# Performance work log

Hardware: AMD Instinct MI355X
Metric: run time of the kernel (lower is better)

## Reference

```python
import jax, jax.numpy as jnp
import numpy as np

BIN = (4, 4)
BN_EPS = 1e-5


def patch_split(t, bin_size):
    # b c (bh rh) (bw rw) -> b (bh bw) rh rw c
    B, C, H, W = t.shape
    bh, bw = bin_size
    rH, rW = H // bh, W // bw
    t = t.reshape(B, C, bh, rH, bw, rW)
    t = jnp.transpose(t, (0, 2, 4, 3, 5, 1))
    return t.reshape(B, bh * bw, rH, rW, C)


def patch_recover(t, bin_size):
    # b (bh bw) rh rw c -> b c (bh rh) (bw rw)
    B, N, rH, rW, C = t.shape
    bh, bw = bin_size
    t = t.reshape(B, bh, bw, rH, rW, C)
    t = jnp.transpose(t, (0, 5, 1, 3, 2, 4))
    return t.reshape(B, C, bh * rH, bw * rW)


def setup_inputs() -> dict:
    key = jax.random.key(0)
    ks = jax.random.split(key, 12)
    B, C, H, W = 4, 512, 128, 128
    Ci = C // 2
    bins = BIN[0] * BIN[1]
    s = lambda fan: 1.0 / np.sqrt(fan)
    return {
        "x": jax.random.normal(ks[0], (B, C, H, W), jnp.float32),
        "w_cam": jax.random.normal(ks[1], (C, C), jnp.float32) * s(C),
        "b_cam": jnp.zeros((C,), jnp.float32),
        "w_gcn1": jax.random.normal(ks[2], (bins, bins), jnp.float32) * s(bins),
        "w_gcn2": jax.random.normal(ks[3], (C, C), jnp.float32) * s(C),
        "w_fuse": jax.random.normal(ks[4], (bins,), jnp.float32) * s(bins),
        "b_fuse": jnp.zeros((1,), jnp.float32),
        "w_q": jax.random.normal(ks[5], (Ci, C), jnp.float32) * s(C),
        "b_q": jnp.zeros((Ci,), jnp.float32),
        "w_k": jax.random.normal(ks[6], (Ci, C), jnp.float32) * s(C),
        "b_k": jnp.zeros((Ci,), jnp.float32),
        "w_v": jax.random.normal(ks[7], (Ci, C), jnp.float32) * s(C),
        "b_v": jnp.zeros((Ci,), jnp.float32),
        "w_out": jax.random.normal(ks[8], (C, Ci), jnp.float32) * s(Ci),
        "bn_gamma": jnp.ones((C,), jnp.float32),
        "bn_beta": jnp.zeros((C,), jnp.float32),
        "bn_mean": jnp.zeros((C,), jnp.float32),
        "bn_var": jnp.ones((C,), jnp.float32),
    }


def reference(x, w_cam, b_cam, w_gcn1, w_gcn2, w_fuse, b_fuse,
              w_q, b_q, w_k, b_k, w_v, b_v, w_out,
              bn_gamma, bn_beta, bn_mean, bn_var):
    B, C, H, W = x.shape
    bh, bw = BIN
    bins = bh * bw
    rH, rW = H // bh, W // bw
    P = rH * rW
    K = w_cam.shape[0]  # num_classes == C

    # conv_cam: 1x1 conv (dropout is identity in eval mode)
    cam = jnp.einsum('bchw,kc->bkhw', x, w_cam) + b_cam[None, :, None, None]

    # adaptive avg pool to (bh, bw) then sigmoid
    pooled = cam.reshape(B, K, bh, rH, bw, rW).mean(axis=(3, 5))  # [B,K,bh,bw]
    cls_score = jax.nn.sigmoid(pooled)

    residual = x
    cam_p = patch_split(cam, BIN).reshape(B, bins, P, K)
    x_p = patch_split(x, BIN).reshape(B, bins, P, C)

    # bin confidence: [B, bins, K, 1]
    bin_conf = jnp.transpose(cls_score.reshape(B, K, bins), (0, 2, 1))[..., None]
    pixel_conf = jax.nn.softmax(cam_p, axis=2)  # softmax over pixels in bin

    # local_feats: [B, bins, K, C]
    local = jnp.einsum('bnpk,bnpc->bnkc', pixel_conf, x_p) * bin_conf

    # GCN over bin (node) dimension
    g = jnp.einsum('nm,bmkc->bnkc', w_gcn1, local)
    g = jax.nn.relu(g + local)
    local_feats = jnp.einsum('bnkc,dc->bnkd', g, w_gcn2)

    # fuse: 1x1 conv bins->1, relu -> global feats [B, K, C]
    glob = jnp.einsum('m,bmkc->bkc', w_fuse, local_feats) + b_fuse[0]
    glob = jax.nn.relu(glob)

    # QKV (no scale applied in original forward)
    query = jnp.einsum('bnpc,ic->bnpi', x_p, w_q) + b_q
    key_t = jnp.einsum('bnkc,ic->bnki', local_feats, w_k) + b_k
    value = jnp.einsum('bkc,ic->bki', glob, w_v) + b_v  # shared across bins

    aff = jnp.einsum('bnpi,bnki->bnpk', query, key_t)
    aff = jax.nn.softmax(aff, axis=-1)
    out = jnp.einsum('bnpk,bki->bnpi', aff, value)  # [B, bins, P, Ci]

    Ci = value.shape[-1]
    out = out.reshape(B, bins, rH, rW, Ci)
    out = patch_recover(out, BIN)  # [B, Ci, H, W]

    # conv_out: 1x1 conv (no bias) + BN (eval) + ReLU
    y = jnp.einsum('bihw,ci->bchw', out, w_out)
    inv = jax.lax.rsqrt(bn_var + BN_EPS)
    y = (y - bn_mean[None, :, None, None]) * (bn_gamma * inv)[None, :, None, None] \
        + bn_beta[None, :, None, None]
    y = jax.nn.relu(y)
    return residual + y
```

## Files before the change

### kernel.cpp

```cpp
#include <hip/hip_runtime.h>
#include <hip/hip_bf16.h>
#include <stdint.h>


typedef __attribute__((ext_vector_type(8))) short bfrag;
typedef __attribute__((ext_vector_type(4))) float ffrag;
typedef __hip_bfloat16 bf16;

__device__ __forceinline__ void load_lds16(const void* g, void* l) {
    __builtin_amdgcn_global_load_lds(
        (const __attribute__((address_space(1))) void*)(uintptr_t)g,
        (__attribute__((address_space(3))) void*)(uintptr_t)l,
        16, 0, 0);
}

__global__ void __launch_bounds__(256) gemm_bf16(
    const short* __restrict__ A, int aBatch,
    const short* __restrict__ B, int bBatch, int bShift,
    short* __restrict__ C, int cBatch,
    int M, int N, int K,
    const float* __restrict__ biasM, const float* __restrict__ biasN,
    const float* __restrict__ scaleM)
{
    __shared__ short As[128 * 64];
    __shared__ short Bs[128 * 64];
    const int t = threadIdx.x;
    const int w = t >> 6, lane = t & 63;
    const int bt = blockIdx.z;
    const int m0 = blockIdx.y * 128, n0 = blockIdx.x * 128;
    const short* gA = A + (size_t)bt * aBatch;
    const short* gB = B + (size_t)(bt >> bShift) * bBatch;
    const int wm = w >> 1, wn = w & 1;

    ffrag acc[4][4] = {};

    const int rowbase = w * 32;
    const int lr = lane >> 3;
    const int lc = lane & 7;

    for (int k0 = 0; k0 < K; k0 += 64) {
#pragma unroll
        for (int j = 0; j < 4; ++j) {
            const int rr = rowbase + j * 8 + lr;
            const int ch = lc ^ (rr & 7);
            load_lds16(gA + (size_t)(m0 + rr) * K + k0 + ch * 8,
                       &As[(rowbase + j * 8) * 64]);
            load_lds16(gB + (size_t)(n0 + rr) * K + k0 + ch * 8,
                       &Bs[(rowbase + j * 8) * 64]);
        }
        __syncthreads();
#pragma unroll
        for (int kk = 0; kk < 2; ++kk) {
            bfrag af[4], bfv[4];
#pragma unroll
            for (int i = 0; i < 4; ++i) {
                const int ra = wm * 64 + i * 16 + (lane & 15);
                const int cl = kk * 4 + (lane >> 4);
                af[i]  = *(const bfrag*)&As[ra * 64 + ((cl ^ (ra & 7)) * 8)];
                const int rb = wn * 64 + i * 16 + (lane & 15);
                bfv[i] = *(const bfrag*)&Bs[rb * 64 + ((cl ^ (rb & 7)) * 8)];
            }
#pragma unroll
            for (int i = 0; i < 4; ++i)
#pragma unroll
                for (int j = 0; j < 4; ++j)
                    acc[i][j] = __builtin_amdgcn_mfma_f32_16x16x32_bf16(
                        af[i], bfv[j], acc[i][j], 0, 0, 0);
        }
        __syncthreads();
    }

    bf16* gC = (bf16*)(C + (size_t)bt * cBatch);
#pragma unroll
    for (int i = 0; i < 4; ++i) {
#pragma unroll
        for (int j = 0; j < 4; ++j) {
            const int col = n0 + wn * 64 + j * 16 + (lane & 15);
            const float bnv = biasN ? biasN[col] : 0.f;
#pragma unroll
            for (int r = 0; r < 4; ++r) {
                const int row = m0 + wm * 64 + i * 16 + (lane >> 4) * 4 + r;
                float v = acc[i][j][r] + bnv + (biasM ? biasM[row] : 0.f);
                if (scaleM) v *= scaleM[bt * M + row];
                gC[(size_t)row * N + col] = __float2bfloat16(v);
            }
        }
    }
}

__global__ void __launch_bounds__(256) wconv(
    const float* __restrict__ wc, const float* __restrict__ wg2,
    const float* __restrict__ wq, const float* __restrict__ wk,
    const float* __restrict__ wv, const float* __restrict__ wo,
    bf16* __restrict__ dst)
{
    const int i = blockIdx.x * 256 + threadIdx.x;
    const float* s; int o;
    if      (i <  262144) { s = wc;  o = i; }
    else if (i <  524288) { s = wg2; o = i - 262144; }
    else if (i <  655360) { s = wq;  o = i - 524288; }
    else if (i <  786432) { s = wk;  o = i - 655360; }
    else if (i <  917504) { s = wv;  o = i - 786432; }
    else                  { s = wo;  o = i - 917504; }
    dst[i] = __float2bfloat16(s[o]);
}

__global__ void __launch_bounds__(256) convert_x(
    const float* __restrict__ x, bf16* __restrict__ xpc, bf16* __restrict__ xcp)
{
    const int bn = blockIdx.x, ct = blockIdx.y, pt = blockIdx.z;
    const int b = bn >> 4, n = bn & 15;
    const int c0 = ct * 32, p0 = pt * 32;
    const int h = (n >> 2) * 32 + pt;
    const int w0 = (n & 3) * 32;
    __shared__ float tile[32][33];
    const int t = threadIdx.x;
    const int pw = t & 31, ci = t >> 5;
#pragma unroll
    for (int i = 0; i < 4; ++i) {
        const int c = c0 + ci + i * 8;
        const float v = x[(((size_t)b * 512 + c) * 128 + h) * 128 + w0 + pw];
        tile[ci + i * 8][pw] = v;
        xcp[((size_t)bn * 512 + c) * 1024 + p0 + pw] = __float2bfloat16(v);
    }
    __syncthreads();
    const int pi = t >> 5, cc = t & 31;
#pragma unroll
    for (int i = 0; i < 4; ++i) {
        const int p = p0 + pi + i * 8;
        xpc[((size_t)bn * 1024 + p) * 512 + c0 + cc] =
            __float2bfloat16(tile[cc][pi + i * 8]);
    }
}

__global__ void __launch_bounds__(256) softmax_pool_1024(
    bf16* __restrict__ conf, float* __restrict__ binconf)
{
    const int row = blockIdx.x;
    bf16* r = conf + (size_t)row * 1024;
    const int t = threadIdx.x;
    bf16 a[4];
    *(uint2*)a = *(const uint2*)(r + t * 4);
    float f[4];
#pragma unroll
    for (int i = 0; i < 4; ++i) f[i] = __bfloat162float(a[i]);
    float s  = f[0] + f[1] + f[2] + f[3];
    float mx = fmaxf(fmaxf(f[0], f[1]), fmaxf(f[2], f[3]));
#pragma unroll
    for (int off = 32; off > 0; off >>= 1) {
        s += __shfl_down(s, off, 64);
        mx = fmaxf(mx, __shfl_down(mx, off, 64));
    }
    __shared__ float rs[4], rm[4], re[4];
    const int wv = t >> 6, ln = t & 63;
    if (ln == 0) { rs[wv] = s; rm[wv] = mx; }
    __syncthreads();
    const float MX = fmaxf(fmaxf(rm[0], rm[1]), fmaxf(rm[2], rm[3]));
    if (t == 0) {
        const float mean = (rs[0] + rs[1] + rs[2] + rs[3]) * (1.f / 1024.f);
        binconf[row] = 1.f / (1.f + __expf(-mean));
    }
    float e[4];
#pragma unroll
    for (int i = 0; i < 4; ++i) e[i] = __expf(f[i] - MX);
    float es = e[0] + e[1] + e[2] + e[3];
#pragma unroll
    for (int off = 32; off > 0; off >>= 1) es += __shfl_down(es, off, 64);
    if (ln == 0) re[wv] = es;
    __syncthreads();
    const float inv = 1.f / (re[0] + re[1] + re[2] + re[3]);
#pragma unroll
    for (int i = 0; i < 4; ++i) a[i] = __float2bfloat16(e[i] * inv);
    *(uint2*)(r + t * 4) = *(uint2*)a;
}

__global__ void __launch_bounds__(256) softmax_rows_512(bf16* __restrict__ aff)
{
    const int t = threadIdx.x;
    const int wv = t >> 6, ln = t & 63;
    const int row = blockIdx.x * 4 + wv;
    bf16* r = aff + (size_t)row * 512;
    bf16 a[8];
    *(uint4*)a = *(const uint4*)(r + ln * 8);
    float f[8];
#pragma unroll
    for (int i = 0; i < 8; ++i) f[i] = __bfloat162float(a[i]);
    float mx = f[0];
#pragma unroll
    for (int i = 1; i < 8; ++i) mx = fmaxf(mx, f[i]);
#pragma unroll
    for (int off = 32; off > 0; off >>= 1) mx = fmaxf(mx, __shfl_down(mx, off, 64));
    mx = __shfl(mx, 0, 64);
    float es = 0.f;
#pragma unroll
    for (int i = 0; i < 8; ++i) { f[i] = __expf(f[i] - mx); es += f[i]; }
#pragma unroll
    for (int off = 32; off > 0; off >>= 1) es += __shfl_down(es, off, 64);
    es = __shfl(es, 0, 64);
    const float inv = 1.f / es;
#pragma unroll
    for (int i = 0; i < 8; ++i) a[i] = __float2bfloat16(f[i] * inv);
    *(uint4*)(r + ln * 8) = *(uint4*)a;
}

__global__ void __launch_bounds__(256) gcn1_kernel(
    const bf16* __restrict__ localb, bf16* __restrict__ g,
    const float* __restrict__ w_gcn1)
{
    __shared__ float wsm[16][16];
    const int t = threadIdx.x;
    wsm[t >> 4][t & 15] = w_gcn1[t];
    const int idx = blockIdx.x * 256 + t;
    const int b  = idx >> 18;
    const int kc = idx & 262143;
    const bf16* lp = localb + (size_t)b * 4194304 + kc;
    __syncthreads();
    float lv[16];
#pragma unroll
    for (int m = 0; m < 16; ++m) lv[m] = __bfloat162float(lp[m * 262144]);
    bf16* gp = g + (size_t)b * 4194304 + kc;
#pragma unroll
    for (int n = 0; n < 16; ++n) {
        float acc = lv[n];
#pragma unroll
        for (int m = 0; m < 16; ++m) acc = fmaf(wsm[n][m], lv[m], acc);
        gp[n * 262144] = __float2bfloat16(fmaxf(acc, 0.f));
    }
}

__global__ void __launch_bounds__(256) glob_kernel(
    const bf16* __restrict__ lfeats, bf16* __restrict__ glob,
    const float* __restrict__ w_fuse, const float* __restrict__ b_fuse)
{
    const int idx = blockIdx.x * 256 + threadIdx.x;
    const int b  = idx >> 18;
    const int kc = idx & 262143;
    const bf16* lp = lfeats + (size_t)b * 4194304 + kc;
    float acc = b_fuse[0];
#pragma unroll
    for (int m = 0; m < 16; ++m)
        acc = fmaf(w_fuse[m], __bfloat162float(lp[m * 262144]), acc);
    glob[idx] = __float2bfloat16(fmaxf(acc, 0.f));
}

__global__ void __launch_bounds__(256) bn_residual(
    const bf16* __restrict__ y, const float* __restrict__ x,
    float* __restrict__ out,
    const float* __restrict__ gam, const float* __restrict__ bet,
    const float* __restrict__ mu, const float* __restrict__ var)
{
    const int i4 = (blockIdx.x * 256 + threadIdx.x) * 4;
    const int w = i4 & 127, h = (i4 >> 7) & 127, c = (i4 >> 14) & 511, b = i4 >> 23;
    const int p  = (h & 31) * 32 + (w & 31);
    const int bn = b * 16 + ((h >> 5) << 2) + (w >> 5);
    bf16 yv[4];
    *(uint2*)yv = *(const uint2*)(y + ((size_t)bn * 512 + c) * 1024 + p);
    const float4 xv = *(const float4*)(x + i4);
    const float sc = gam[c] * rsqrtf(var[c] + 1e-5f);
    const float mm = mu[c], bb = bet[c];
    float4 o;
    o.x = xv.x + fmaxf(fmaf(__bfloat162float(yv[0]) - mm, sc, bb), 0.f);
    o.y = xv.y + fmaxf(fmaf(__bfloat162float(yv[1]) - mm, sc, bb), 0.f);
    o.z = xv.z + fmaxf(fmaf(__bfloat162float(yv[2]) - mm, sc, bb), 0.f);
    o.w = xv.w + fmaxf(fmaf(__bfloat162float(yv[3]) - mm, sc, bb), 0.f);
    *(float4*)(out + i4) = o;
}

extern "C" void kernel_launch(void* const* d_in, const int* in_sizes, int n_in,
                              void* d_out, int out_size, void* d_ws, size_t ws_size,
                              hipStream_t stream) {
    (void)in_sizes; (void)n_in; (void)out_size; (void)ws_size;
    const float* x      = (const float*)d_in[0];
    const float* w_cam  = (const float*)d_in[1];
    const float* b_cam  = (const float*)d_in[2];
    const float* w_gcn1 = (const float*)d_in[3];
    const float* w_gcn2 = (const float*)d_in[4];
    const float* w_fuse = (const float*)d_in[5];
    const float* b_fuse = (const float*)d_in[6];
    const float* w_q    = (const float*)d_in[7];
    const float* b_q    = (const float*)d_in[8];
    const float* w_k    = (const float*)d_in[9];
    const float* b_k    = (const float*)d_in[10];
    const float* w_v    = (const float*)d_in[11];
    const float* b_v    = (const float*)d_in[12];
    const float* w_out  = (const float*)d_in[13];
    const float* bng    = (const float*)d_in[14];
    const float* bnb    = (const float*)d_in[15];
    const float* bnm    = (const float*)d_in[16];
    const float* bnv    = (const float*)d_in[17];

    char* base = (char*)d_ws;
    bf16*  wbf    = (bf16*)(base);
    float* bc     = (float*)(base + 2097152);
    bf16*  xpc    = (bf16*)(base + 2228224);
    bf16*  xcp    = (bf16*)(base + 69337088);
    bf16*  confb  = (bf16*)(base + 136445952);
    bf16*  localb = (bf16*)(base + 203554816);
    bf16*  g      = xcp;
    bf16*  lf     = (bf16*)(base + 102891520);
    bf16*  globb  = confb;
    bf16*  vt     = (bf16*)(base + 138543104);
    bf16*  key    = (bf16*)(base + 139067392);
    bf16*  query  = (bf16*)(base + 155844608);
    bf16*  aff    = xpc;
    bf16*  attn   = lf;
    bf16*  ybuf   = confb;

    bf16* wcam = wbf;
    bf16* wg2  = wbf + 262144;
    bf16* wq   = wbf + 524288;
    bf16* wk   = wbf + 655360;
    bf16* wv   = wbf + 786432;
    bf16* wo   = wbf + 917504;

    wconv<<<4096, 256, 0, stream>>>(w_cam, w_gcn2, w_q, w_k, w_v, w_out, wbf);
    convert_x<<<dim3(64, 16, 32), 256, 0, stream>>>(x, xpc, xcp);

    gemm_bf16<<<dim3(8, 4, 64), 256, 0, stream>>>(
        (const short*)wcam, 0, (const short*)xpc, 524288, 0,
        (short*)confb, 524288, 512, 1024, 512, b_cam, nullptr, nullptr);
    softmax_pool_1024<<<32768, 256, 0, stream>>>(confb, bc);
    gemm_bf16<<<dim3(4, 4, 64), 256, 0, stream>>>(
        (const short*)confb, 524288, (const short*)xcp, 524288, 0,
        (short*)localb, 262144, 512, 512, 1024, nullptr, nullptr, bc);
    gcn1_kernel<<<4096, 256, 0, stream>>>(localb, g, w_gcn1);
    gemm_bf16<<<dim3(4, 256, 1), 256, 0, stream>>>(
        (const short*)g, 0, (const short*)wg2, 0, 0,
        (short*)lf, 0, 32768, 512, 512, nullptr, nullptr, nullptr);
    glob_kernel<<<4096, 256, 0, stream>>>(lf, globb, w_fuse, b_fuse);
    gemm_bf16<<<dim3(4, 2, 4), 256, 0, stream>>>(
        (const short*)wv, 0, (const short*)globb, 262144, 0,
        (short*)vt, 131072, 256, 512, 512, b_v, nullptr, nullptr);
    gemm_bf16<<<dim3(2, 256, 1), 256, 0, stream>>>(
        (const short*)lf, 0, (const short*)wk, 0, 0,
        (short*)key, 0, 32768, 256, 512, nullptr, b_k, nullptr);
    gemm_bf16<<<dim3(2, 8, 64), 256, 0, stream>>>(
        (const short*)xpc, 524288, (const short*)wq, 0, 0,
        (short*)query, 262144, 1024, 256, 512, nullptr, b_q, nullptr);
    gemm_bf16<<<dim3(4, 8, 64), 256, 0, stream>>>(
        (const short*)query, 262144, (const short*)key, 131072, 0,
        (short*)aff, 524288, 1024, 512, 256, nullptr, nullptr, nullptr);
    softmax_rows_512<<<16384, 256, 0, stream>>>(aff);
    gemm_bf16<<<dim3(2, 8, 64), 256, 0, stream>>>(
        (const short*)aff, 524288, (const short*)vt, 131072, 4,
        (short*)attn, 262144, 1024, 256, 512, nullptr, nullptr, nullptr);
    gemm_bf16<<<dim3(8, 4, 64), 256, 0, stream>>>(
        (const short*)wo, 0, (const short*)attn, 262144, 0,
        (short*)ybuf, 524288, 512, 1024, 256, nullptr, nullptr, nullptr);
    bn_residual<<<32768, 256, 0, stream>>>(ybuf, x, (float*)d_out, bng, bnb, bnm, bnv);
}
```

Measured before the change: 820.5 us.

## Fuse BN+residual epilogue into output GEMM and remap block order for XCD locality

```diff
diff --git a/kernel.cpp b/kernel.cpp
--- a/kernel.cpp
+++ b/kernel.cpp
@@ -14,20 +14,43 @@
         16, 0, 0);
 }
 
+template<int EPI>
 __global__ void __launch_bounds__(256) gemm_bf16(
     const short* __restrict__ A, int aBatch,
     const short* __restrict__ B, int bBatch, int bShift,
     short* __restrict__ C, int cBatch,
-    int M, int N, int K,
+    int M, int N, int K, int mT, int nT, int zTotal,
     const float* __restrict__ biasM, const float* __restrict__ biasN,
-    const float* __restrict__ scaleM)
+    const float* __restrict__ scaleM,
+    const float* __restrict__ xres,
+    const float* __restrict__ bng, const float* __restrict__ bnb,
+    const float* __restrict__ bnm, const float* __restrict__ bnv)
 {
     __shared__ short As[128 * 64];
     __shared__ short Bs[128 * 64];
     const int t = threadIdx.x;
     const int w = t >> 6, lane = t & 63;
-    const int bt = blockIdx.z;
-    const int m0 = blockIdx.y * 128, n0 = blockIdx.x * 128;
+
+    const int id = blockIdx.x;
+    const int T = mT * nT;
+    int bt, mt, nt;
+    if (zTotal >= 8) {
+        const int x = id & 7, q = id >> 3;
+        const int tile = q % T;
+        bt = (q / T) * 8 + x;
+        mt = tile / nT; nt = tile % nT;
+    } else if (zTotal == 1 && (mT & 7) == 0) {
+        const int x = id & 7, q = id >> 3;
+        nt = q % nT;
+        mt = x * (mT >> 3) + q / nT;
+        bt = 0;
+    } else {
+        bt = id / T;
+        const int tile = id % T;
+        mt = tile / nT; nt = tile % nT;
+    }
+    const int m0 = mt * 128, n0 = nt * 128;
+
     const short* gA = A + (size_t)bt * aBatch;
     const short* gB = B + (size_t)(bt >> bShift) * bBatch;
     const int wm = w >> 1, wn = w & 1;
@@ -70,19 +93,43 @@
         __syncthreads();
     }
 
-    bf16* gC = (bf16*)(C + (size_t)bt * cBatch);
-#pragma unroll
-    for (int i = 0; i < 4; ++i) {
-#pragma unroll
-        for (int j = 0; j < 4; ++j) {
-            const int col = n0 + wn * 64 + j * 16 + (lane & 15);
-            const float bnv = biasN ? biasN[col] : 0.f;
+    if (EPI == 0) {
+        bf16* gC = (bf16*)(C + (size_t)bt * cBatch);
+#pragma unroll
+        for (int i = 0; i < 4; ++i) {
+#pragma unroll
+            for (int j = 0; j < 4; ++j) {
+                const int col = n0 + wn * 64 + j * 16 + (lane & 15);
+                const float bnvl = biasN ? biasN[col] : 0.f;
+#pragma unroll
+                for (int r = 0; r < 4; ++r) {
+                    const int row = m0 + wm * 64 + i * 16 + (lane >> 4) * 4 + r;
+                    float v = acc[i][j][r] + bnvl + (biasM ? biasM[row] : 0.f);
+                    if (scaleM) v *= scaleM[bt * M + row];
+                    gC[(size_t)row * N + col] = __float2bfloat16(v);
+                }
+            }
+        }
+    } else {
+        float* O = (float*)C;
+        const int b = bt >> 4, binq = bt & 15;
+        const int h0 = (binq >> 2) * 32, w0 = (binq & 3) * 32;
+#pragma unroll
+        for (int i = 0; i < 4; ++i) {
 #pragma unroll
             for (int r = 0; r < 4; ++r) {
-                const int row = m0 + wm * 64 + i * 16 + (lane >> 4) * 4 + r;
-                float v = acc[i][j][r] + bnv + (biasM ? biasM[row] : 0.f);
-                if (scaleM) v *= scaleM[bt * M + row];
-                gC[(size_t)row * N + col] = __float2bfloat16(v);
+                const int c = m0 + wm * 64 + i * 16 + (lane >> 4) * 4 + r;
+                const float sc = bng[c] * rsqrtf(bnv[c] + 1e-5f);
+                const float mm = bnm[c], bb = bnb[c];
+#pragma unroll
+                for (int j = 0; j < 4; ++j) {
+                    const int p = n0 + wn * 64 + j * 16 + (lane & 15);
+                    const size_t flat =
+                        (((size_t)b * 512 + c) * 128 + h0 + (p >> 5)) * 128
+                        + w0 + (p & 31);
+                    O[flat] = xres[flat]
+                        + fmaxf(fmaf(acc[i][j][r] - mm, sc, bb), 0.f);
+                }
             }
         }
     }
@@ -241,29 +288,6 @@
     for (int m = 0; m < 16; ++m)
         acc = fmaf(w_fuse[m], __bfloat162float(lp[m * 262144]), acc);
     glob[idx] = __float2bfloat16(fmaxf(acc, 0.f));
-}
-
-__global__ void __launch_bounds__(256) bn_residual(
-    const bf16* __restrict__ y, const float* __restrict__ x,
-    float* __restrict__ out,
-    const float* __restrict__ gam, const float* __restrict__ bet,
-    const float* __restrict__ mu, const float* __restrict__ var)
-{
-    const int i4 = (blockIdx.x * 256 + threadIdx.x) * 4;
-    const int w = i4 & 127, h = (i4 >> 7) & 127, c = (i4 >> 14) & 511, b = i4 >> 23;
-    const int p  = (h & 31) * 32 + (w & 31);
-    const int bn = b * 16 + ((h >> 5) << 2) + (w >> 5);
-    bf16 yv[4];
-    *(uint2*)yv = *(const uint2*)(y + ((size_t)bn * 512 + c) * 1024 + p);
-    const float4 xv = *(const float4*)(x + i4);
-    const float sc = gam[c] * rsqrtf(var[c] + 1e-5f);
-    const float mm = mu[c], bb = bet[c];
-    float4 o;
-    o.x = xv.x + fmaxf(fmaf(__bfloat162float(yv[0]) - mm, sc, bb), 0.f);
-    o.y = xv.y + fmaxf(fmaf(__bfloat162float(yv[1]) - mm, sc, bb), 0.f);
-    o.z = xv.z + fmaxf(fmaf(__bfloat162float(yv[2]) - mm, sc, bb), 0.f);
-    o.w = xv.w + fmaxf(fmaf(__bfloat162float(yv[3]) - mm, sc, bb), 0.f);
-    *(float4*)(out + i4) = o;
 }
 
 extern "C" void kernel_launch(void* const* d_in, const int* in_sizes, int n_in,
@@ -304,7 +328,6 @@
     bf16*  query  = (bf16*)(base + 155844608);
     bf16*  aff    = xpc;
     bf16*  attn   = lf;
-    bf16*  ybuf   = confb;
 
     bf16* wcam = wbf;
     bf16* wg2  = wbf + 262144;
@@ -316,36 +339,44 @@
     wconv<<<4096, 256, 0, stream>>>(w_cam, w_gcn2, w_q, w_k, w_v, w_out, wbf);
     convert_x<<<dim3(64, 16, 32), 256, 0, stream>>>(x, xpc, xcp);
 
-    gemm_bf16<<<dim3(8, 4, 64), 256, 0, stream>>>(
+    gemm_bf16<0><<<4 * 8 * 64, 256, 0, stream>>>(
         (const short*)wcam, 0, (const short*)xpc, 524288, 0,
-        (short*)confb, 524288, 512, 1024, 512, b_cam, nullptr, nullptr);
+        (short*)confb, 524288, 512, 1024, 512, 4, 8, 64,
+        b_cam, nullptr, nullptr, nullptr, nullptr, nullptr, nullptr, nullptr);
     softmax_pool_1024<<<32768, 256, 0, stream>>>(confb, bc);
-    gemm_bf16<<<dim3(4, 4, 64), 256, 0, stream>>>(
+    gemm_bf16<0><<<4 * 4 * 64, 256, 0, stream>>>(
         (const short*)confb, 524288, (const short*)xcp, 524288, 0,
-        (short*)localb, 262144, 512, 512, 1024, nullptr, nullptr, bc);
+        (short*)localb, 262144, 512, 512, 1024, 4, 4, 64,
+        nullptr, nullptr, bc, nullptr, nullptr, nullptr, nullptr, nullptr);
     gcn1_kernel<<<4096, 256, 0, stream>>>(localb, g, w_gcn1);
-    gemm_bf16<<<dim3(4, 256, 1), 256, 0, stream>>>(
+    gemm_bf16<0><<<256 * 4, 256, 0, stream>>>(
         (const short*)g, 0, (const short*)wg2, 0, 0,
-        (short*)lf, 0, 32768, 512, 512, nullptr, nullptr, nullptr);
+        (short*)lf, 0, 32768, 512, 512, 256, 4, 1,
+        nullptr, nullptr, nullptr, nullptr, nullptr, nullptr, nullptr, nullptr);
     glob_kernel<<<4096, 256, 0, stream>>>(lf, globb, w_fuse, b_fuse);
-    gemm_bf16<<<dim3(4, 2, 4), 256, 0, stream>>>(
+    gemm_bf16<0><<<2 * 4 * 4, 256, 0, stream>>>(
         (const short*)wv, 0, (const short*)globb, 262144, 0,
-        (short*)vt, 131072, 256, 512, 512, b_v, nullptr, nullptr);
-    gemm_bf16<<<dim3(2, 256, 1), 256, 0, stream>>>(
+        (short*)vt, 131072, 256, 512, 512, 2, 4, 4,
+        b_v, nullptr, nullptr, nullptr, nullptr, nullptr, nullptr, nullptr);
+    gemm_bf16<0><<<256 * 2, 256, 0, stream>>>(
         (const short*)lf, 0, (const short*)wk, 0, 0,
-        (short*)key, 0, 32768, 256, 512, nullptr, b_k, nullptr);
-    gemm_bf16<<<dim3(2, 8, 64), 256, 0, stream>>>(
+        (short*)key, 0, 32768, 256, 512, 256, 2, 1,
+        nullptr, b_k, nullptr, nullptr, nullptr, nullptr, nullptr, nullptr);
+    gemm_bf16<0><<<8 * 2 * 64, 256, 0, stream>>>(
         (const short*)xpc, 524288, (const short*)wq, 0, 0,
-        (short*)query, 262144, 1024, 256, 512, nullptr, b_q, nullptr);
-    gemm_bf16<<<dim3(4, 8, 64), 256, 0, stream>>>(
+        (short*)query, 262144, 1024, 256, 512, 8, 2, 64,
+        nullptr, b_q, nullptr, nullptr, nullptr, nullptr, nullptr, nullptr);
+    gemm_bf16<0><<<8 * 4 * 64, 256, 0, stream>>>(
         (const short*)query, 262144, (const short*)key, 131072, 0,
-        (short*)aff, 524288, 1024, 512, 256, nullptr, nullptr, nullptr);
+        (short*)aff, 524288, 1024, 512, 256, 8, 4, 64,
+        nullptr, nullptr, nullptr, nullptr, nullptr, nullptr, nullptr, nullptr);
     softmax_rows_512<<<16384, 256, 0, stream>>>(aff);
-    gemm_bf16<<<dim3(2, 8, 64), 256, 0, stream>>>(
+    gemm_bf16<0><<<8 * 2 * 64, 256, 0, stream>>>(
         (const short*)aff, 524288, (const short*)vt, 131072, 4,
-        (short*)attn, 262144, 1024, 256, 512, nullptr, nullptr, nullptr);
-    gemm_bf16<<<dim3(8, 4, 64), 256, 0, stream>>>(
+        (short*)attn, 262144, 1024, 256, 512, 8, 2, 64,
+        nullptr, nullptr, nullptr, nullptr, nullptr, nullptr, nullptr, nullptr);
+    gemm_bf16<1><<<4 * 8 * 64, 256, 0, stream>>>(
         (const short*)wo, 0, (const short*)attn, 262144, 0,
-        (short*)ybuf, 524288, 512, 1024, 256, nullptr, nullptr, nullptr);
-    bn_residual<<<32768, 256, 0, stream>>>(ybuf, x, (float*)d_out, bng, bnb, bnm, bnv);
-}
+        (short*)d_out, 0, 512, 1024, 256, 4, 8, 64,
+        nullptr, nullptr, nullptr, x, bng, bnb, bnm, bnv);
+}
```

Result: faster. 769.4 us (-6.2%).
